# Optimization experiments

Measured on AMD Instinct MI355X. Metric: run time of the kernel, lower is better.

The kernel has to match this reference:

```python
import jax, jax.numpy as jnp
import numpy as np

BETA = 0.95
THRESHOLD = 1.0
NUM_STEPS = 255

# snntorch Heaviside spike with ATan surrogate gradient (alpha=2):
# forward: (x > 0), backward: g / (1 + (pi*x)^2)
@jax.custom_vjp
def heaviside_atan(x):
    return (x > 0).astype(x.dtype)

def _h_fwd(x):
    return heaviside_atan(x), x

def _h_bwd(x, g):
    return (g / (1.0 + (jnp.pi * x) ** 2),)

heaviside_atan.defvjp(_h_fwd, _h_bwd)


def setup_inputs() -> dict:
    key = jax.random.key(0)
    k1, k2 = jax.random.split(key)
    x = jax.random.normal(k1, (65536, 784), dtype=jnp.float32)
    W = jax.random.normal(k2, (1, 784), dtype=jnp.float32) * 0.035  # ~1/sqrt(784)
    return {"x": x, "W": W}


def reference(x, W):
    # fc(x) is identical every step -> compute once (same math as the loop)
    cur = x @ W.T  # [B, 1]
    mem0 = jnp.zeros_like(cur)

    def step(mem, _):
        # snntorch Leaky, reset_mechanism='zero':
        # reset computed from PREVIOUS membrane, then decay+input, zeroed on reset
        reset = heaviside_atan(mem - THRESHOLD)
        mem_new = (BETA * mem + cur) * (1.0 - reset)
        spk = heaviside_atan(mem_new - THRESHOLD)
        return mem_new, (spk, mem_new)

    _, (spk_rec, mem_rec) = jax.lax.scan(step, mem0, None, length=NUM_STEPS)
    # spk_rec, mem_rec: [NUM_STEPS, B, 1] -- matches torch.stack(dim=0)
    return spk_rec, mem_rec
```

## Files before the change

kernel.cpp:

```cpp
#include <hip/hip_runtime.h>


#define NROWS   65536
#define DIM     784
#define STEPS   255
#define BETA    0.95
#define ROWS_PB 64

__global__ __launch_bounds__(64) void snn_fused(const float* __restrict__ x,
                                                const float* __restrict__ W,
                                                float* __restrict__ out) {
    __shared__ double cur_s[ROWS_PB];
    const int lane = threadIdx.x;
    const long long rowBase = (long long)blockIdx.x * ROWS_PB;

    const float4* __restrict__ W4 = (const float4*)W;
    const float4 w0 = W4[lane];
    const float4 w1 = W4[lane + 64];
    const float4 w2 = W4[lane + 128];
    float4 w3 = make_float4(0.f, 0.f, 0.f, 0.f);
    if (lane < 4) w3 = W4[192 + lane];

    #pragma unroll 4
    for (int r = 0; r < ROWS_PB; ++r) {
        const float4* __restrict__ xr = (const float4*)(x + (rowBase + r) * DIM);
        float4 a0 = xr[lane];
        float4 a1 = xr[lane + 64];
        float4 a2 = xr[lane + 128];
        float4 a3 = make_float4(0.f, 0.f, 0.f, 0.f);
        if (lane < 4) a3 = xr[192 + lane];

        double s = (double)a0.x * (double)w0.x + (double)a0.y * (double)w0.y
                 + (double)a0.z * (double)w0.z + (double)a0.w * (double)w0.w
                 + (double)a1.x * (double)w1.x + (double)a1.y * (double)w1.y
                 + (double)a1.z * (double)w1.z + (double)a1.w * (double)w1.w
                 + (double)a2.x * (double)w2.x + (double)a2.y * (double)w2.y
                 + (double)a2.z * (double)w2.z + (double)a2.w * (double)w2.w
                 + (double)a3.x * (double)w3.x + (double)a3.y * (double)w3.y
                 + (double)a3.z * (double)w3.z + (double)a3.w * (double)w3.w;

        #pragma unroll
        for (int off = 32; off > 0; off >>= 1)
            s += __shfl_down(s, off, 64);
        if (lane == 0) cur_s[r] = s;
    }
    __syncthreads();

    const double cur = cur_s[lane];
    double mem = 0.0;
    float* __restrict__ spkOut = out;
    float* __restrict__ memOut = out + (long long)STEPS * NROWS;
    long long idx = rowBase + lane;

    for (int t = 0; t < STEPS; ++t) {
        const double m = BETA * mem + cur;
        mem = (mem > 1.0) ? 0.0 : m;
        spkOut[idx] = (mem > 1.0) ? 1.0f : 0.0f;
        memOut[idx] = (float)mem;
        idx += NROWS;
    }
}

extern "C" void kernel_launch(void* const* d_in, const int* in_sizes, int n_in,
                              void* d_out, int out_size, void* d_ws, size_t ws_size,
                              hipStream_t stream) {
    const float* x = (const float*)d_in[0];
    const float* W = (const float*)d_in[1];
    float* out = (float*)d_out;

    dim3 grid(NROWS / ROWS_PB);
    dim3 block(ROWS_PB);
    hipLaunchKernelGGL(snn_fused, grid, block, 0, stream, x, W, out);
}
```

Measured before the change: 334.1 us.

## Split fused kernel into parallel matvec and recurrence kernels with nontemporal stores

Splits the single fused kernel, which had one 64-thread wave per block looping serially over 64 rows, into two kernels. The first computes the dot products with one wave per row and 4 rows per 256-thread block, writing them to a double workspace. The second runs the 255-step recurrence with 256 threads per block and writes spike and membrane outputs with nontemporal stores. This raises occupancy and memory-level parallelism for both phases, at the cost of a second launch and a small round trip through global memory for the workspace.

```diff
diff --git a/kernel.cpp b/kernel.cpp
--- a/kernel.cpp
+++ b/kernel.cpp
@@ -5,59 +5,58 @@
 #define DIM     784
 #define STEPS   255
 #define BETA    0.95
-#define ROWS_PB 64
 
-__global__ __launch_bounds__(64) void snn_fused(const float* __restrict__ x,
-                                                const float* __restrict__ W,
-                                                float* __restrict__ out) {
-    __shared__ double cur_s[ROWS_PB];
-    const int lane = threadIdx.x;
-    const long long rowBase = (long long)blockIdx.x * ROWS_PB;
+__global__ __launch_bounds__(256) void snn_matvec(const float* __restrict__ x,
+                                                  const float* __restrict__ W,
+                                                  double* __restrict__ cur) {
+    const int lane = threadIdx.x & 63;
+    const long long row = (long long)blockIdx.x * 4 + (threadIdx.x >> 6);
 
     const float4* __restrict__ W4 = (const float4*)W;
-    const float4 w0 = W4[lane];
-    const float4 w1 = W4[lane + 64];
-    const float4 w2 = W4[lane + 128];
+    const float4* __restrict__ xr = (const float4*)(x + row * DIM);
+
+    float4 a0 = xr[lane];
+    float4 a1 = xr[lane + 64];
+    float4 a2 = xr[lane + 128];
+    float4 w0 = W4[lane];
+    float4 w1 = W4[lane + 64];
+    float4 w2 = W4[lane + 128];
+    float4 a3 = make_float4(0.f, 0.f, 0.f, 0.f);
     float4 w3 = make_float4(0.f, 0.f, 0.f, 0.f);
-    if (lane < 4) w3 = W4[192 + lane];
+    if (lane < 4) { a3 = xr[192 + lane]; w3 = W4[192 + lane]; }
 
-    #pragma unroll 4
-    for (int r = 0; r < ROWS_PB; ++r) {
-        const float4* __restrict__ xr = (const float4*)(x + (rowBase + r) * DIM);
-        float4 a0 = xr[lane];
-        float4 a1 = xr[lane + 64];
-        float4 a2 = xr[lane + 128];
-        float4 a3 = make_float4(0.f, 0.f, 0.f, 0.f);
-        if (lane < 4) a3 = xr[192 + lane];
+    double s = (double)a0.x * (double)w0.x + (double)a0.y * (double)w0.y
+             + (double)a0.z * (double)w0.z + (double)a0.w * (double)w0.w
+             + (double)a1.x * (double)w1.x + (double)a1.y * (double)w1.y
+             + (double)a1.z * (double)w1.z + (double)a1.w * (double)w1.w
+             + (double)a2.x * (double)w2.x + (double)a2.y * (double)w2.y
+             + (double)a2.z * (double)w2.z + (double)a2.w * (double)w2.w
+             + (double)a3.x * (double)w3.x + (double)a3.y * (double)w3.y
+             + (double)a3.z * (double)w3.z + (double)a3.w * (double)w3.w;
 
-        double s = (double)a0.x * (double)w0.x + (double)a0.y * (double)w0.y
-                 + (double)a0.z * (double)w0.z + (double)a0.w * (double)w0.w
-                 + (double)a1.x * (double)w1.x + (double)a1.y * (double)w1.y
-                 + (double)a1.z * (double)w1.z + (double)a1.w * (double)w1.w
-                 + (double)a2.x * (double)w2.x + (double)a2.y * (double)w2.y
-                 + (double)a2.z * (double)w2.z + (double)a2.w * (double)w2.w
-                 + (double)a3.x * (double)w3.x + (double)a3.y * (double)w3.y
-                 + (double)a3.z * (double)w3.z + (double)a3.w * (double)w3.w;
+    #pragma unroll
+    for (int off = 32; off > 0; off >>= 1)
+        s += __shfl_down(s, off, 64);
 
-        #pragma unroll
-        for (int off = 32; off > 0; off >>= 1)
-            s += __shfl_down(s, off, 64);
-        if (lane == 0) cur_s[r] = s;
-    }
-    __syncthreads();
+    if (lane == 0) cur[row] = s;
+}
 
-    const double cur = cur_s[lane];
+__global__ __launch_bounds__(256) void snn_recur(const double* __restrict__ curBuf,
+                                                 float* __restrict__ out) {
+    const long long row = (long long)blockIdx.x * blockDim.x + threadIdx.x;
+    const double cur = curBuf[row];
     double mem = 0.0;
-    float* __restrict__ spkOut = out;
-    float* __restrict__ memOut = out + (long long)STEPS * NROWS;
-    long long idx = rowBase + lane;
+
+    float* __restrict__ spkOut = out + row;
+    float* __restrict__ memOut = out + (long long)STEPS * NROWS + row;
 
     for (int t = 0; t < STEPS; ++t) {
         const double m = BETA * mem + cur;
         mem = (mem > 1.0) ? 0.0 : m;
-        spkOut[idx] = (mem > 1.0) ? 1.0f : 0.0f;
-        memOut[idx] = (float)mem;
-        idx += NROWS;
+        __builtin_nontemporal_store((mem > 1.0) ? 1.0f : 0.0f, spkOut);
+        __builtin_nontemporal_store((float)mem, memOut);
+        spkOut += NROWS;
+        memOut += NROWS;
     }
 }
 
@@ -67,8 +66,8 @@
     const float* x = (const float*)d_in[0];
     const float* W = (const float*)d_in[1];
     float* out = (float*)d_out;
+    double* cur = (double*)d_ws;
 
-    dim3 grid(NROWS / ROWS_PB);
-    dim3 block(ROWS_PB);
-    hipLaunchKernelGGL(snn_fused, grid, block, 0, stream, x, W, out);
+    hipLaunchKernelGGL(snn_matvec, dim3(NROWS / 4), dim3(256), 0, stream, x, W, cur);
+    hipLaunchKernelGGL(snn_recur, dim3(NROWS / 256), dim3(256), 0, stream, cur, out);
 }
```

After: 313.1 us. 1.07x faster.
